# Kernel tuning notes

Hardware: AMD Instinct MI355X
Metric: run time of the kernel (lower is better)

The kernel has to match this reference:

```python
import jax, jax.numpy as jnp
import numpy as np

NQ, NK, D = 8192, 8192, 256
NEG_INF = -1e30


def setup_inputs() -> dict:
    key = jax.random.key(0)
    kK, kV, kQ, kM = jax.random.split(key, 4)
    K = jax.random.normal(kK, (NK, D), dtype=jnp.float32)
    V = jax.random.normal(kV, (NK, D), dtype=jnp.float32)
    Q = jax.random.normal(kQ, (NQ, D), dtype=jnp.float32)
    m = jax.random.randint(kM, (NQ, NK), 0, 2) > 0  # bool mask, True = attend
    return {"K": K, "V": V, "Q": Q, "m": m}


def reference(K, V, Q, m):
    # affinity: scaled dot product with optional mask
    scale = 1.0 / jnp.sqrt(jnp.asarray(D, dtype=Q.dtype))
    QKt = jnp.einsum('qd,kd->qk', Q, K) * scale  # [NQ, NK]
    QKt = jnp.where(m, QKt, NEG_INF)
    # normalization: softmax over keys
    QKt_n = jax.nn.softmax(QKt, axis=-1)
    # weighted sum of values
    return QKt_n @ V  # [NQ, D]
```

## Files before the change

kernel.cpp:

```cpp
#include <hip/hip_runtime.h>
#include <stdint.h>
#include <stddef.h>

#define NQS 8192
#define NKS 8192
#define DS  256

typedef _Float16 half8 __attribute__((ext_vector_type(8)));
typedef _Float16 half4v __attribute__((ext_vector_type(4)));
typedef float floatx16 __attribute__((ext_vector_type(16)));
typedef float floatx4e __attribute__((ext_vector_type(4)));
typedef uint32_t uint32x4 __attribute__((ext_vector_type(4)));

#define MFMA32(A,B,C) __builtin_amdgcn_mfma_f32_32x32x16_f16(A,B,C,0,0,0)

#define GLOAD_LDS16(gp, lp) \
  __builtin_amdgcn_global_load_lds((const __attribute__((address_space(1))) void*)(gp), \
                                   (__attribute__((address_space(3))) void*)(lp), 16, 0, 0)

#define TILE_ELEMS 16384
#define SUB_ELEMS  8192

__global__ void prep(const float* __restrict__ Qf, const float* __restrict__ K,
                     const float* __restrict__ V, const uint8_t* __restrict__ Msk,
                     _Float16* __restrict__ Qh, _Float16* __restrict__ Kc,
                     _Float16* __restrict__ Vc, uint32_t* __restrict__ flag){
  __shared__ uint32_t sdet[256];
  const int tid = threadIdx.x;
  const int bid = blockIdx.x;
  if (bid == 0){
    const uint4* M4 = (const uint4*)Msk;
    uint32_t acc = 0;
    for (int i = tid; i < 4096; i += 256){
      uint4 v = M4[i];
      acc |= v.x | v.y | v.z | v.w;
    }
    sdet[tid] = acc;
    __syncthreads();
    if (tid == 0){
      uint32_t t = 0;
      for (int i = 0; i < 256; i++) t |= sdet[i];
      *flag = (t > 1u) ? 1u : 0u;
    }
    return;
  }
  if (bid <= 1024){
    size_t u = (size_t)(bid - 1)*256 + tid;
    const float4* src = (const float4*)(Qf + u*8);
    float4 a = src[0], b = src[1];
    half8 h = {(_Float16)a.x,(_Float16)a.y,(_Float16)a.z,(_Float16)a.w,
               (_Float16)b.x,(_Float16)b.y,(_Float16)b.z,(_Float16)b.w};
    *(half8*)(Qh + u*8) = h;
  } else if (bid <= 2048){
    int gid = (bid - 1025)*256 + tid;
    int key = gid & 8191;
    int c   = gid >> 13;
    int kt = c >> 1, t = c & 1;
    const float4* s = (const float4*)(K + (size_t)key*DS + kt*16 + t*8);
    float4 x = s[0], y = s[1];
    half8 h = {(_Float16)x.x,(_Float16)x.y,(_Float16)x.z,(_Float16)x.w,
               (_Float16)y.x,(_Float16)y.y,(_Float16)y.z,(_Float16)y.w};
    int tile = key >> 6, mt = (key >> 5) & 1, k32 = key & 31;
    size_t off = (size_t)tile*TILE_ELEMS + (((mt*16 + kt)*2 + t)*32 + k32)*8;
    *(half8*)(Kc + off) = h;
  } else {
    int gid = (bid - 2049)*256 + tid;
    int d32 = gid & 31;
    int t   = (gid >> 5) & 1;
    int nt  = (gid >> 6) & 7;
    int kkt = (gid >> 9) & 3;
    int tile = gid >> 11;
    int d = nt*32 + d32;
    int kb8 = tile*64 + kkt*16 + t*8;
    half8 h;
    #pragma unroll
    for (int j=0;j<8;j++) h[j] = (_Float16)V[(size_t)(kb8 + j)*DS + d];
    *(half8*)(Vc + (size_t)gid*8) = h;
  }
}

__global__ __launch_bounds__(256, 2) void attn_fwd(
  const _Float16* __restrict__ Qh, const _Float16* __restrict__ Kc,
  const _Float16* __restrict__ Vc, const uint8_t* __restrict__ Msk,
  const uint32_t* __restrict__ flag, _Float16* __restrict__ Oph,
  float* __restrict__ Lo)
{
  __shared__ _Float16 Kls[2][SUB_ELEMS];
  __shared__ _Float16 Vls[2][SUB_ELEMS];
  __shared__ uint8_t  Pk[16][128][8];

  const int tid  = threadIdx.x;
  const int w    = tid >> 6;
  const int lane = tid & 63;
  const int q32  = lane & 31;
  const int t    = lane >> 5;
  const int b    = blockIdx.x;
  const int kh   = b & 7;
  const int rb   = (b >> 3)*128;
  const int rowbase = rb + w*32;
  const int sub0 = kh << 5;
  const int kbase = kh << 10;

  const float kLog = 0.09016844005556021f;
  const float MFIX = 6.0f;

  const bool bm = (*flag != 0u);

  {
    const size_t base = (size_t)sub0 * SUB_ELEMS;
    #pragma unroll
    for (int j=0;j<4;j++){
      int c = w*4 + j;
      GLOAD_LDS16(Kc + base + c*512 + lane*8, &Kls[0][c*512]);
      GLOAD_LDS16(Vc + base + c*512 + lane*8, &Vls[0][c*512]);
    }
  }

  if (bm){
    const uint8_t* mrow = Msk + (size_t)(rb + (tid>>1))*NKS + kbase + (tid&1)*16;
    #pragma unroll 1
    for (int sp=0; sp<16; ++sp){
      uint32x4 e = __builtin_nontemporal_load((const uint32x4*)(mrow + sp*64));
      uint32x4 o = __builtin_nontemporal_load((const uint32x4*)(mrow + sp*64 + 32));
      uint32_t w4 = 0;
      #pragma unroll
      for (int q=0;q<4;q++){
        uint32_t xe = e[q], xo = o[q];
        uint32_t ne = ((xe&0x000000FFu)?1u:0u)|((xe&0x0000FF00u)?2u:0u)|
                      ((xe&0x00FF0000u)?4u:0u)|((xe&0xFF000000u)?8u:0u);
        uint32_t no = ((xo&0x000000FFu)?1u:0u)|((xo&0x0000FF00u)?2u:0u)|
                      ((xo&0x00FF0000u)?4u:0u)|((xo&0xFF000000u)?8u:0u);
        w4 |= (ne | (no << 4)) << (8*q);
      }
      *(uint32_t*)&Pk[sp][tid>>1][(tid&1)*4] = w4;
    }
  } else {
    const uint32_t* M32 = (const uint32_t*)Msk;
    #pragma unroll 1
    for (int sp=0; sp<16; ++sp){
      uint32x4 e[4], o[4];
      #pragma unroll
      for (int jj=0;jj<4;jj++){
        const uint32_t* p = M32 + (size_t)(rb + jj*32 + (tid>>3))*NKS + kbase + sp*64 + (tid&7)*4;
        e[jj] = __builtin_nontemporal_load((const uint32x4*)p);
        o[jj] = __builtin_nontemporal_load((const uint32x4*)(p + 32));
      }
      #pragma unroll
      for (int jj=0;jj<4;jj++){
        uint8_t ne = (uint8_t)((e[jj][0]?1u:0u)|(e[jj][1]?2u:0u)|(e[jj][2]?4u:0u)|(e[jj][3]?8u:0u));
        uint8_t no = (uint8_t)((o[jj][0]?1u:0u)|(o[jj][1]?2u:0u)|(o[jj][2]?4u:0u)|(o[jj][3]?8u:0u));
        Pk[sp][jj*32 + (tid>>3)][tid&7] = (uint8_t)(ne | (no << 4));
      }
    }
  }

  half8 qf[16];
  {
    const _Float16* qrow = Qh + (size_t)(rowbase + q32)*DS;
    #pragma unroll
    for (int kt=0;kt<16;kt++)
      qf[kt] = *(const half8*)(qrow + kt*16 + t*8);
  }

  floatx16 O[8];
  #pragma unroll
  for (int nt=0;nt<8;nt++)
    #pragma unroll
    for (int i=0;i<16;i++) O[nt][i] = 0.f;
  float ls[4] = {0.f, 0.f, 0.f, 0.f};

  __syncthreads();

  #pragma unroll 1
  for (int it=0; it<32; ++it){
    const int buf = it & 1;

    if (it < 31){
      const size_t base = (size_t)(sub0 + it + 1) * SUB_ELEMS;
      #pragma unroll
      for (int j=0;j<4;j++){
        int c = w*4 + j;
        GLOAD_LDS16(Kc + base + c*512 + lane*8, &Kls[buf^1][c*512]);
        GLOAD_LDS16(Vc + base + c*512 + lane*8, &Vls[buf^1][c*512]);
      }
    }

    const uint2 nq = *(const uint2*)&Pk[it>>1][w*32 + q32][0];
    const int sh = (it & 1) * 4;
    const uint32_t nib_s[4] = { (nq.x >> (8*t + sh))      & 0xFu,
                                (nq.x >> (16 + 8*t + sh)) & 0xFu,
                                (nq.y >> (8*t + sh))      & 0xFu,
                                (nq.y >> (16 + 8*t + sh)) & 0xFu };

    floatx16 S0, S1;
    #pragma unroll
    for (int i=0;i<16;i++){ S0[i]=0.f; S1[i]=0.f; }
    __builtin_amdgcn_s_setprio(1);
    #pragma unroll
    for (int kt=0;kt<8;kt++){
      half8 kA0 = *(const half8*)&Kls[buf][((kt*2 + t)*32 + q32)*8];
      half8 kA1 = *(const half8*)&Kls[buf][(((kt+8)*2 + t)*32 + q32)*8];
      S0 = MFMA32(kA0, qf[kt],   S0);
      S1 = MFMA32(kA1, qf[kt+8], S1);
    }
    __builtin_amdgcn_s_setprio(0);

    uint32_t pk[4][2];
    #pragma unroll
    for (int s=0;s<4;s++){
      float pv[4];
      #pragma unroll
      for (int rr=0;rr<4;rr++){
        int i = s*4 + rr;
        float e = __builtin_amdgcn_exp2f(__builtin_fmaf(S0[i]+S1[i], kLog, -MFIX));
        float p = ((nib_s[s] >> rr) & 1u) ? e : 0.f;
        ls[s] += p;
        pv[rr] = p;
      }
      pk[s][0] = __builtin_bit_cast(uint32_t, __builtin_amdgcn_cvt_pkrtz(pv[0], pv[1]));
      pk[s][1] = __builtin_bit_cast(uint32_t, __builtin_amdgcn_cvt_pkrtz(pv[2], pv[3]));
    }

    #pragma unroll
    for (int kt2=0; kt2<2; ++kt2){
      const int s_own  = kt2*2 + t;
      const int s_send = kt2*2 + (t^1);
      uint32_t r0 = __shfl_xor(__builtin_bit_cast(int, pk[s_send][0]), 32);
      uint32_t r1 = __shfl_xor(__builtin_bit_cast(int, pk[s_send][1]), 32);
      uint32_t lo0 = (t==0) ? pk[s_own][0] : r0;
      uint32_t lo1 = (t==0) ? pk[s_own][1] : r1;
      uint32_t hi0 = (t==0) ? r0 : pk[s_own][0];
      uint32_t hi1 = (t==0) ? r1 : pk[s_own][1];
      uint4 u = {lo0, lo1, hi0, hi1};
      half8 pa = __builtin_bit_cast(half8, u);
      __builtin_amdgcn_s_setprio(1);
      #pragma unroll
      for (int nt=0;nt<8;nt++){
        half8 vB = *(const half8*)&Vls[buf][(((kt2*8+nt)*2 + t)*32 + q32)*8];
        O[nt] = MFMA32(pa, vB, O[nt]);
      }
      __builtin_amdgcn_s_setprio(0);
    }

    __syncthreads();
  }

  float lsum = (ls[0] + ls[1]) + (ls[2] + ls[3]);
  lsum += __builtin_bit_cast(float, __shfl_xor(__builtin_bit_cast(int, lsum), 32));
  if (t == 0) __builtin_nontemporal_store(lsum, &Lo[(size_t)b*128 + w*32 + q32]);

  _Float16* ob = Oph + ((size_t)b*128 + w*32)*256;
  #pragma unroll
  for (int nt=0;nt<8;nt++){
    #pragma unroll
    for (int i=0;i<16;i++){
      int row = (i&3) + 8*(i>>2) + 4*t;
      __builtin_nontemporal_store((_Float16)O[nt][i], &ob[(size_t)row*256 + nt*32 + q32]);
    }
  }
}

__global__ void combine8(const _Float16* __restrict__ Oph, const float* __restrict__ Lo,
                         float* __restrict__ Out){
  int gid = blockIdx.x*256 + threadIdx.x;
  int row = gid >> 5;
  int c8  = (gid & 31) << 3;
  int g   = row >> 7, r = row & 127;

  float lt = 0.f;
  #pragma unroll
  for (int kh=0;kh<8;kh++) lt += __builtin_nontemporal_load(&Lo[(size_t)(g*8 + kh)*128 + r]);
  float li = 1.0f / lt;

  float acc[8] = {0.f,0.f,0.f,0.f,0.f,0.f,0.f,0.f};
  #pragma unroll
  for (int kh=0;kh<8;kh++){
    half8 o = __builtin_nontemporal_load(
        (const half8*)(Oph + ((size_t)(g*8 + kh)*128 + r)*256 + c8));
    #pragma unroll
    for (int j=0;j<8;j++) acc[j] += (float)o[j];
  }
  floatx4e a0 = {acc[0]*li, acc[1]*li, acc[2]*li, acc[3]*li};
  floatx4e a1 = {acc[4]*li, acc[5]*li, acc[6]*li, acc[7]*li};
  __builtin_nontemporal_store(a0, (floatx4e*)(Out + (size_t)row*DS + c8));
  __builtin_nontemporal_store(a1, (floatx4e*)(Out + (size_t)row*DS + c8 + 4));
}

extern "C" void kernel_launch(void* const* d_in, const int* in_sizes, int n_in,
                              void* d_out, int out_size, void* d_ws, size_t ws_size,
                              hipStream_t stream){
  (void)in_sizes; (void)n_in; (void)out_size; (void)ws_size;
  const float*   K = (const float*)d_in[0];
  const float*   V = (const float*)d_in[1];
  const float*   Q = (const float*)d_in[2];
  const uint8_t* M = (const uint8_t*)d_in[3];
  float* Out = (float*)d_out;

  _Float16* Qh  = (_Float16*)d_ws;
  _Float16* Kc  = Qh + (size_t)NQS*DS;
  _Float16* Vc  = Kc + (size_t)NKS*DS;
  _Float16* Oph = Vc + (size_t)NKS*DS;
  float*    Lo  = (float*)(Oph + (size_t)512*128*256);
  uint32_t* flag = (uint32_t*)(Lo + 512*128);

  hipLaunchKernelGGL(prep,     dim3(3073), dim3(256), 0, stream, Q, K, V, M, Qh, Kc, Vc, flag);
  hipLaunchKernelGGL(attn_fwd, dim3(512),  dim3(256), 0, stream, Qh, Kc, Vc, M, flag, Oph, Lo);
  hipLaunchKernelGGL(combine8, dim3(1024), dim3(256), 0, stream, Oph, Lo, Out);
}
```

Measured before the change: 471.8 us.

## Software-pipeline QK^T of the next tile with PV of the current tile

Restructures the main loop so the QK^T MFMAs for tile s+1 are interleaved with the PV MFMAs for tile s, with a prologue and an epilogue added. K and V staging are split so V(s+1) and K(s+2) are issued at the top of each iteration, behind a barrier. The intent is to keep the matrix units busy with independent accumulator chains while the softmax exp and packing for a tile run, hiding MFMA dependency latency. In exchange the S accumulators for the next tile stay live across iterations, which raises register pressure, and the loop body and tail code are duplicated.

```diff
diff --git a/kernel.cpp b/kernel.cpp
--- a/kernel.cpp
+++ b/kernel.cpp
@@ -106,15 +106,27 @@
 
   const bool bm = (*flag != 0u);
 
-  {
-    const size_t base = (size_t)sub0 * SUB_ELEMS;
+  auto STAGE_K = [&](int s){
+    const size_t base = (size_t)(sub0 + s) * SUB_ELEMS;
+    _Float16* dst = &Kls[s & 1][0];
     #pragma unroll
     for (int j=0;j<4;j++){
       int c = w*4 + j;
-      GLOAD_LDS16(Kc + base + c*512 + lane*8, &Kls[0][c*512]);
-      GLOAD_LDS16(Vc + base + c*512 + lane*8, &Vls[0][c*512]);
-    }
-  }
+      GLOAD_LDS16(Kc + base + c*512 + lane*8, dst + c*512);
+    }
+  };
+  auto STAGE_V = [&](int s){
+    const size_t base = (size_t)(sub0 + s) * SUB_ELEMS;
+    _Float16* dst = &Vls[s & 1][0];
+    #pragma unroll
+    for (int j=0;j<4;j++){
+      int c = w*4 + j;
+      GLOAD_LDS16(Vc + base + c*512 + lane*8, dst + c*512);
+    }
+  };
+
+  STAGE_K(0);
+  STAGE_V(0);
 
   if (bm){
     const uint8_t* mrow = Msk + (size_t)(rb + (tid>>1))*NKS + kbase + (tid&1)*16;
@@ -169,58 +181,54 @@
     for (int i=0;i<16;i++) O[nt][i] = 0.f;
   float ls[4] = {0.f, 0.f, 0.f, 0.f};
 
+  floatx16 S0, S1;
+
   __syncthreads();
 
+  STAGE_K(1);
+  {
+    #pragma unroll
+    for (int i=0;i<16;i++){ S0[i]=0.f; S1[i]=0.f; }
+    __builtin_amdgcn_s_setprio(1);
+    #pragma unroll
+    for (int kt=0;kt<8;kt++){
+      half8 kA0 = *(const half8*)&Kls[0][((kt*2 + t)*32 + q32)*8];
+      half8 kA1 = *(const half8*)&Kls[0][(((kt+8)*2 + t)*32 + q32)*8];
+      S0 = MFMA32(kA0, qf[kt],   S0);
+      S1 = MFMA32(kA1, qf[kt+8], S1);
+    }
+    __builtin_amdgcn_s_setprio(0);
+  }
+
   #pragma unroll 1
-  for (int it=0; it<32; ++it){
-    const int buf = it & 1;
-
-    if (it < 31){
-      const size_t base = (size_t)(sub0 + it + 1) * SUB_ELEMS;
-      #pragma unroll
-      for (int j=0;j<4;j++){
-        int c = w*4 + j;
-        GLOAD_LDS16(Kc + base + c*512 + lane*8, &Kls[buf^1][c*512]);
-        GLOAD_LDS16(Vc + base + c*512 + lane*8, &Vls[buf^1][c*512]);
-      }
-    }
-
-    const uint2 nq = *(const uint2*)&Pk[it>>1][w*32 + q32][0];
-    const int sh = (it & 1) * 4;
+  for (int s=0; s<31; ++s){
+    __syncthreads();
+    STAGE_V(s+1);
+    if (s < 30) STAGE_K(s+2);
+
+    const uint2 nq = *(const uint2*)&Pk[s>>1][w*32 + q32][0];
+    const int sh = (s & 1) * 4;
     const uint32_t nib_s[4] = { (nq.x >> (8*t + sh))      & 0xFu,
                                 (nq.x >> (16 + 8*t + sh)) & 0xFu,
                                 (nq.y >> (8*t + sh))      & 0xFu,
                                 (nq.y >> (16 + 8*t + sh)) & 0xFu };
-
-    floatx16 S0, S1;
-    #pragma unroll
-    for (int i=0;i<16;i++){ S0[i]=0.f; S1[i]=0.f; }
-    __builtin_amdgcn_s_setprio(1);
-    #pragma unroll
-    for (int kt=0;kt<8;kt++){
-      half8 kA0 = *(const half8*)&Kls[buf][((kt*2 + t)*32 + q32)*8];
-      half8 kA1 = *(const half8*)&Kls[buf][(((kt+8)*2 + t)*32 + q32)*8];
-      S0 = MFMA32(kA0, qf[kt],   S0);
-      S1 = MFMA32(kA1, qf[kt+8], S1);
-    }
-    __builtin_amdgcn_s_setprio(0);
-
     uint32_t pk[4][2];
     #pragma unroll
-    for (int s=0;s<4;s++){
+    for (int sg=0;sg<4;sg++){
       float pv[4];
       #pragma unroll
       for (int rr=0;rr<4;rr++){
-        int i = s*4 + rr;
+        int i = sg*4 + rr;
         float e = __builtin_amdgcn_exp2f(__builtin_fmaf(S0[i]+S1[i], kLog, -MFIX));
-        float p = ((nib_s[s] >> rr) & 1u) ? e : 0.f;
-        ls[s] += p;
+        float p = ((nib_s[sg] >> rr) & 1u) ? e : 0.f;
+        ls[sg] += p;
         pv[rr] = p;
       }
-      pk[s][0] = __builtin_bit_cast(uint32_t, __builtin_amdgcn_cvt_pkrtz(pv[0], pv[1]));
-      pk[s][1] = __builtin_bit_cast(uint32_t, __builtin_amdgcn_cvt_pkrtz(pv[2], pv[3]));
-    }
-
+      pk[sg][0] = __builtin_bit_cast(uint32_t, __builtin_amdgcn_cvt_pkrtz(pv[0], pv[1]));
+      pk[sg][1] = __builtin_bit_cast(uint32_t, __builtin_amdgcn_cvt_pkrtz(pv[2], pv[3]));
+    }
+
+    half8 pa[2];
     #pragma unroll
     for (int kt2=0; kt2<2; ++kt2){
       const int s_own  = kt2*2 + t;
@@ -232,17 +240,75 @@
       uint32_t hi0 = (t==0) ? r0 : pk[s_own][0];
       uint32_t hi1 = (t==0) ? r1 : pk[s_own][1];
       uint4 u = {lo0, lo1, hi0, hi1};
-      half8 pa = __builtin_bit_cast(half8, u);
-      __builtin_amdgcn_s_setprio(1);
-      #pragma unroll
-      for (int nt=0;nt<8;nt++){
-        half8 vB = *(const half8*)&Vls[buf][(((kt2*8+nt)*2 + t)*32 + q32)*8];
-        O[nt] = MFMA32(pa, vB, O[nt]);
-      }
-      __builtin_amdgcn_s_setprio(0);
-    }
-
+      pa[kt2] = __builtin_bit_cast(half8, u);
+    }
+
+    const int nb = (s+1) & 1, cb = s & 1;
+    #pragma unroll
+    for (int i=0;i<16;i++){ S0[i]=0.f; S1[i]=0.f; }
+    __builtin_amdgcn_s_setprio(1);
+    #pragma unroll
+    for (int kt=0;kt<8;kt++){
+      half8 kA0 = *(const half8*)&Kls[nb][((kt*2 + t)*32 + q32)*8];
+      half8 kA1 = *(const half8*)&Kls[nb][(((kt+8)*2 + t)*32 + q32)*8];
+      half8 vB0 = *(const half8*)&Vls[cb][((kt*2 + t)*32 + q32)*8];
+      half8 vB1 = *(const half8*)&Vls[cb][(((8+kt)*2 + t)*32 + q32)*8];
+      S0    = MFMA32(kA0, qf[kt],   S0);
+      O[kt] = MFMA32(pa[0], vB0,   O[kt]);
+      S1    = MFMA32(kA1, qf[kt+8], S1);
+      O[kt] = MFMA32(pa[1], vB1,   O[kt]);
+    }
+    __builtin_amdgcn_s_setprio(0);
+  }
+
+  {
+    const int s = 31;
     __syncthreads();
+    const uint2 nq = *(const uint2*)&Pk[s>>1][w*32 + q32][0];
+    const int sh = (s & 1) * 4;
+    const uint32_t nib_s[4] = { (nq.x >> (8*t + sh))      & 0xFu,
+                                (nq.x >> (16 + 8*t + sh)) & 0xFu,
+                                (nq.y >> (8*t + sh))      & 0xFu,
+                                (nq.y >> (16 + 8*t + sh)) & 0xFu };
+    uint32_t pk[4][2];
+    #pragma unroll
+    for (int sg=0;sg<4;sg++){
+      float pv[4];
+      #pragma unroll
+      for (int rr=0;rr<4;rr++){
+        int i = sg*4 + rr;
+        float e = __builtin_amdgcn_exp2f(__builtin_fmaf(S0[i]+S1[i], kLog, -MFIX));
+        float p = ((nib_s[sg] >> rr) & 1u) ? e : 0.f;
+        ls[sg] += p;
+        pv[rr] = p;
+      }
+      pk[sg][0] = __builtin_bit_cast(uint32_t, __builtin_amdgcn_cvt_pkrtz(pv[0], pv[1]));
+      pk[sg][1] = __builtin_bit_cast(uint32_t, __builtin_amdgcn_cvt_pkrtz(pv[2], pv[3]));
+    }
+    half8 pa[2];
+    #pragma unroll
+    for (int kt2=0; kt2<2; ++kt2){
+      const int s_own  = kt2*2 + t;
+      const int s_send = kt2*2 + (t^1);
+      uint32_t r0 = __shfl_xor(__builtin_bit_cast(int, pk[s_send][0]), 32);
+      uint32_t r1 = __shfl_xor(__builtin_bit_cast(int, pk[s_send][1]), 32);
+      uint32_t lo0 = (t==0) ? pk[s_own][0] : r0;
+      uint32_t lo1 = (t==0) ? pk[s_own][1] : r1;
+      uint32_t hi0 = (t==0) ? r0 : pk[s_own][0];
+      uint32_t hi1 = (t==0) ? r1 : pk[s_own][1];
+      uint4 u = {lo0, lo1, hi0, hi1};
+      pa[kt2] = __builtin_bit_cast(half8, u);
+    }
+    const int cb = s & 1;
+    __builtin_amdgcn_s_setprio(1);
+    #pragma unroll
+    for (int kt=0;kt<8;kt++){
+      half8 vB0 = *(const half8*)&Vls[cb][((kt*2 + t)*32 + q32)*8];
+      half8 vB1 = *(const half8*)&Vls[cb][(((8+kt)*2 + t)*32 + q32)*8];
+      O[kt] = MFMA32(pa[0], vB0, O[kt]);
+      O[kt] = MFMA32(pa[1], vB1, O[kt]);
+    }
+    __builtin_amdgcn_s_setprio(0);
   }
 
   float lsum = (ls[0] + ls[1]) + (ls[2] + ls[3]);
```

After: 477.9 us. About the same (+1.3%).

## Load K/V fragments directly from global into registers, dropping LDS double-buffering

Applied to the files above, without the earlier changes.

Removes the shared-memory double buffer for K and V sub-tiles and their async global-to-LDS loads. Each wave now reads its MFMA operand fragments for every sub-tile straight from global memory into registers. The goal is to free LDS so that launch bounds can rise to four blocks per CU, and to reduce barriers to one every eight iterations. In exchange, every wave in a block fetches the same K/V data separately, which multiplies L2 traffic. There is no prefetch, so load latency is exposed each iteration, and the extra register arrays risk spills under the tighter register budget.

```diff
diff --git a/kernel.cpp b/kernel.cpp
--- a/kernel.cpp
+++ b/kernel.cpp
@@ -13,10 +13,6 @@
 typedef uint32_t uint32x4 __attribute__((ext_vector_type(4)));
 
 #define MFMA32(A,B,C) __builtin_amdgcn_mfma_f32_32x32x16_f16(A,B,C,0,0,0)
-
-#define GLOAD_LDS16(gp, lp) \
-  __builtin_amdgcn_global_load_lds((const __attribute__((address_space(1))) void*)(gp), \
-                                   (__attribute__((address_space(3))) void*)(lp), 16, 0, 0)
 
 #define TILE_ELEMS 16384
 #define SUB_ELEMS  8192
@@ -79,15 +75,13 @@
   }
 }
 
-__global__ __launch_bounds__(256, 2) void attn_fwd(
+__global__ __launch_bounds__(256, 4) void attn_fwd(
   const _Float16* __restrict__ Qh, const _Float16* __restrict__ Kc,
   const _Float16* __restrict__ Vc, const uint8_t* __restrict__ Msk,
   const uint32_t* __restrict__ flag, _Float16* __restrict__ Oph,
   float* __restrict__ Lo)
 {
-  __shared__ _Float16 Kls[2][SUB_ELEMS];
-  __shared__ _Float16 Vls[2][SUB_ELEMS];
-  __shared__ uint8_t  Pk[16][128][8];
+  __shared__ uint8_t Pk[16][128][8];
 
   const int tid  = threadIdx.x;
   const int w    = tid >> 6;
@@ -106,16 +100,6 @@
 
   const bool bm = (*flag != 0u);
 
-  {
-    const size_t base = (size_t)sub0 * SUB_ELEMS;
-    #pragma unroll
-    for (int j=0;j<4;j++){
-      int c = w*4 + j;
-      GLOAD_LDS16(Kc + base + c*512 + lane*8, &Kls[0][c*512]);
-      GLOAD_LDS16(Vc + base + c*512 + lane*8, &Vls[0][c*512]);
-    }
-  }
-
   if (bm){
     const uint8_t* mrow = Msk + (size_t)(rb + (tid>>1))*NKS + kbase + (tid&1)*16;
     #pragma unroll 1
@@ -172,21 +156,19 @@
   __syncthreads();
 
   #pragma unroll 1
-  for (int it=0; it<32; ++it){
-    const int buf = it & 1;
-
-    if (it < 31){
-      const size_t base = (size_t)(sub0 + it + 1) * SUB_ELEMS;
-      #pragma unroll
-      for (int j=0;j<4;j++){
-        int c = w*4 + j;
-        GLOAD_LDS16(Kc + base + c*512 + lane*8, &Kls[buf^1][c*512]);
-        GLOAD_LDS16(Vc + base + c*512 + lane*8, &Vls[buf^1][c*512]);
-      }
-    }
-
-    const uint2 nq = *(const uint2*)&Pk[it>>1][w*32 + q32][0];
-    const int sh = (it & 1) * 4;
+  for (int s=0; s<32; ++s){
+    const _Float16* kvb = Kc + (size_t)(sub0 + s) * SUB_ELEMS;
+    const _Float16* vvb = Vc + (size_t)(sub0 + s) * SUB_ELEMS;
+
+    half8 ka[16];
+    #pragma unroll
+    for (int i=0;i<16;i++) ka[i] = *(const half8*)(kvb + (size_t)(i*64 + lane)*8);
+    half8 vb[16];
+    #pragma unroll
+    for (int i=0;i<16;i++) vb[i] = *(const half8*)(vvb + (size_t)(i*64 + lane)*8);
+
+    const uint2 nq = *(const uint2*)&Pk[s>>1][w*32 + q32][0];
+    const int sh = (s & 1) * 4;
     const uint32_t nib_s[4] = { (nq.x >> (8*t + sh))      & 0xFu,
                                 (nq.x >> (16 + 8*t + sh)) & 0xFu,
                                 (nq.y >> (8*t + sh))      & 0xFu,
@@ -198,29 +180,28 @@
     __builtin_amdgcn_s_setprio(1);
     #pragma unroll
     for (int kt=0;kt<8;kt++){
-      half8 kA0 = *(const half8*)&Kls[buf][((kt*2 + t)*32 + q32)*8];
-      half8 kA1 = *(const half8*)&Kls[buf][(((kt+8)*2 + t)*32 + q32)*8];
-      S0 = MFMA32(kA0, qf[kt],   S0);
-      S1 = MFMA32(kA1, qf[kt+8], S1);
+      S0 = MFMA32(ka[kt],   qf[kt],   S0);
+      S1 = MFMA32(ka[kt+8], qf[kt+8], S1);
     }
     __builtin_amdgcn_s_setprio(0);
 
     uint32_t pk[4][2];
     #pragma unroll
-    for (int s=0;s<4;s++){
+    for (int sg=0;sg<4;sg++){
       float pv[4];
       #pragma unroll
       for (int rr=0;rr<4;rr++){
-        int i = s*4 + rr;
+        int i = sg*4 + rr;
         float e = __builtin_amdgcn_exp2f(__builtin_fmaf(S0[i]+S1[i], kLog, -MFIX));
-        float p = ((nib_s[s] >> rr) & 1u) ? e : 0.f;
-        ls[s] += p;
+        float p = ((nib_s[sg] >> rr) & 1u) ? e : 0.f;
+        ls[sg] += p;
         pv[rr] = p;
       }
-      pk[s][0] = __builtin_bit_cast(uint32_t, __builtin_amdgcn_cvt_pkrtz(pv[0], pv[1]));
-      pk[s][1] = __builtin_bit_cast(uint32_t, __builtin_amdgcn_cvt_pkrtz(pv[2], pv[3]));
-    }
-
+      pk[sg][0] = __builtin_bit_cast(uint32_t, __builtin_amdgcn_cvt_pkrtz(pv[0], pv[1]));
+      pk[sg][1] = __builtin_bit_cast(uint32_t, __builtin_amdgcn_cvt_pkrtz(pv[2], pv[3]));
+    }
+
+    half8 pa[2];
     #pragma unroll
     for (int kt2=0; kt2<2; ++kt2){
       const int s_own  = kt2*2 + t;
@@ -232,17 +213,20 @@
       uint32_t hi0 = (t==0) ? r0 : pk[s_own][0];
       uint32_t hi1 = (t==0) ? r1 : pk[s_own][1];
       uint4 u = {lo0, lo1, hi0, hi1};
-      half8 pa = __builtin_bit_cast(half8, u);
-      __builtin_amdgcn_s_setprio(1);
+      pa[kt2] = __builtin_bit_cast(half8, u);
+    }
+
+    __builtin_amdgcn_s_setprio(1);
+    #pragma unroll
+    for (int kt2=0; kt2<2; ++kt2){
       #pragma unroll
       for (int nt=0;nt<8;nt++){
-        half8 vB = *(const half8*)&Vls[buf][(((kt2*8+nt)*2 + t)*32 + q32)*8];
-        O[nt] = MFMA32(pa, vB, O[nt]);
-      }
-      __builtin_amdgcn_s_setprio(0);
-    }
-
-    __syncthreads();
+        O[nt] = MFMA32(pa[kt2], vb[kt2*8 + nt], O[nt]);
+      }
+    }
+    __builtin_amdgcn_s_setprio(0);
+
+    if ((s & 7) == 7) __syncthreads();
   }
 
   float lsum = (ls[0] + ls[1]) + (ls[2] + ls[3]);
```

Result: slower. 1.663 ms (+252.5%).
